# Performance work log

Hardware: AMD Instinct MI355X
Metric: run time of the kernel (lower is better)

Reference implementation:

```python
import jax, jax.numpy as jnp
import numpy as np

NUM_NODES = 512

def chebyshev_convolution(laplacian, signal, weights, t0):
    # Faithful port of the torch helper, including tk_prev staying equal to
    # `laplacian` throughout the loop (as in the source).
    k = weights.shape[0]
    # t0 is the identity, so t0 @ signal == signal
    out = jnp.matmul(signal, weights[0])
    out = out + jnp.matmul(jnp.matmul(laplacian, signal), weights[1])
    tk_prev = laplacian
    tk = 2.0 * jnp.matmul(laplacian, laplacian) - t0
    for i in range(2, k):
        out = out + jnp.matmul(jnp.matmul(tk, signal), weights[i])
        tk = 2.0 * jnp.matmul(laplacian, tk) - tk_prev
    return out


def setup_inputs() -> dict:
    key = jax.random.key(0)
    ks = jax.random.split(key, 5)
    B, T, N, C_IN, C_OUT, CS, CD = 4, 12, NUM_NODES, 64, 64, 3, 6
    std_l = 0.1 / np.sqrt(N)
    std_t = 0.1 / np.sqrt(C_IN)
    x = jax.random.normal(ks[0], (B, T, N, C_IN), dtype=jnp.float32)
    ws = jax.random.uniform(ks[1], (N, N), jnp.float32, -std_l, std_l)
    ts = jax.random.uniform(ks[2], (CS, C_IN, C_OUT), jnp.float32, -std_t, std_t)
    wp = jax.random.uniform(ks[3], (C_IN, C_IN), jnp.float32, -std_t, std_t)
    td = jax.random.uniform(ks[4], (CD, C_IN, C_OUT), jnp.float32, -std_t, std_t)
    return {"x": x, "ws": ws, "ts": ts, "wp": wp, "td": td}


def reference(x, ws, ts, wp, td):
    N = NUM_NODES
    t0 = jnp.eye(N, dtype=x.dtype)
    # Static (SGC) branch: Chebyshev conv with learned static Laplacian ws
    out_s = chebyshev_convolution(ws, x, ts, t0)
    # Dynamic branch: data-dependent Laplacian wd = x @ (wp @ x^T)  -> (B,T,N,N)
    wd = jnp.matmul(x, jnp.matmul(wp, jnp.swapaxes(x, -2, -1)))
    wd = wd + jnp.min(wd)
    wd = wd / jnp.max(wd) / (N ** 2)
    out_d = chebyshev_convolution(wd, x, td, t0)
    return out_s + out_d
```

## Files before the change

### kernel.cpp

```cpp
#include <hip/hip_runtime.h>
#include <cstddef>
#include <cstdint>

#define NN 512
#define CC 64
#define BT 48

typedef __bf16 bf16_t;
typedef bf16_t bf16x8 __attribute__((ext_vector_type(8)));
typedef bf16_t bf16x4 __attribute__((ext_vector_type(4)));
typedef float f32x4 __attribute__((ext_vector_type(4)));

#define OFF_MN    0
#define OFF_MX    384
#define OFF_WSB   1024
#define OFF_WS2B  132096
#define OFF_XBT   263168
#define OFF_XNB   1049600
#define OFF_XNR   1836032
#define OFF_CS0   2622464
#define OFF_T1T   2647040
#define OFF_T2T   2649088
#define OFF_Z1N   2651136
#define OFF_Z2N   3437568
#define OFF_WEB   4224000
#define OFF_WER   4322304
#define OFF_VDY   4420608

__device__ __forceinline__ f32x4 mfma(bf16x8 a, bf16x8 b, f32x4 c) {
  return __builtin_amdgcn_mfma_f32_16x16x32_bf16(a, b, c, 0, 0, 0);
}
__device__ __forceinline__ int swz_chunk(int r, int c8) {
  return r * 64 + ((c8 ^ (r & 7)) << 3);
}
__device__ __forceinline__ int swz_e(int r, int c) {
  return r * 64 + ((((c >> 3) ^ (r & 7)) << 3)) + (c & 7);
}
__device__ __forceinline__ bf16x8 frag(const bf16_t* sm, int row, int kc) {
  return *(const bf16x8*)(sm + row * 64 + ((kc ^ (row & 7)) << 3));
}
__device__ __forceinline__ void stage64(bf16_t* sm, const bf16_t* g, int ld, int tid) {
#pragma unroll
  for (int j = 0; j < 2; ++j) {
    int id = tid + 256 * j;
    int r = id >> 3, c8 = id & 7;
    bf16x8 v = *(const bf16x8*)(g + (size_t)r * ld + c8 * 8);
    *(bf16x8*)(sm + swz_chunk(r, c8)) = v;
  }
}
__device__ __forceinline__ void stage64f(bf16_t* sm, const float* g, int ld, int tid) {
#pragma unroll
  for (int j = 0; j < 4; ++j) {
    int idx = tid + 256 * j;
    int r = idx >> 4, cc = (idx & 15) * 4;
    float4 v = *(const float4*)(g + (size_t)r * ld + cc);
    bf16x4 o = {(bf16_t)v.x, (bf16_t)v.y, (bf16_t)v.z, (bf16_t)v.w};
    *(bf16x4*)(sm + swz_e(r, cc)) = o;
  }
}
struct bfpair { bf16_t b, r; };
__device__ __forceinline__ bfpair splitbf(float f) {
  bfpair p;
  p.b = (bf16_t)f;
  p.r = (bf16_t)(f - (float)p.b);
  return p;
}

__global__ __launch_bounds__(256) void k_pre(
    const float* __restrict__ x, const float* __restrict__ wsL,
    const float* __restrict__ ts, const float* __restrict__ wp,
    float* __restrict__ wsf)
{
  __shared__ __align__(16) char pool[32768];
  __shared__ float red[16];
  const int tid = threadIdx.x;
  const int b = blockIdx.x;
  const int w = tid >> 6, l = tid & 63, lh = l >> 4, lr = l & 15, m0 = w * 16;

  if (b < 384) {
    const int bt = (b & 7) + 8 * (b >> 6);
    const int it = (b >> 3) & 7;
    const int i0 = it * 64;
    float (*XsF)[66] = (float(*)[66])pool;
    bf16_t* XBT = (bf16_t*)(wsf + OFF_XBT);
    bf16_t* XNb = (bf16_t*)(wsf + OFF_XNB);
    bf16_t* XNr = (bf16_t*)(wsf + OFF_XNR);
    float* CS0 = wsf + OFF_CS0;
    const float* xg = x + ((size_t)bt * NN + i0) * CC;
    for (int j = 0; j < 4; ++j) {
      int idx = tid + 256 * j;
      int r = idx >> 4, c0v = (idx & 15) * 4;
      float4 v = *(const float4*)(xg + (size_t)r * CC + c0v);
      bfpair p0 = splitbf(v.x), p1 = splitbf(v.y), p2 = splitbf(v.z), p3 = splitbf(v.w);
      bf16x4 vb = {p0.b, p1.b, p2.b, p3.b};
      bf16x4 vr = {p0.r, p1.r, p2.r, p3.r};
      size_t gb = ((size_t)bt * 512 + i0 + r) * 64 + c0v;
      *(bf16x4*)(XNb + gb) = vb;
      *(bf16x4*)(XNr + gb) = vr;
      XsF[c0v + 0][r] = v.x; XsF[c0v + 1][r] = v.y;
      XsF[c0v + 2][r] = v.z; XsF[c0v + 3][r] = v.w;
    }
    __syncthreads();
    {
      int c = tid >> 2, k0 = (tid & 3) * 16;
      bf16x8 o1, o2;
#pragma unroll
      for (int q = 0; q < 8; ++q) {
        o1[q] = (bf16_t)XsF[c][k0 + q];
        o2[q] = (bf16_t)XsF[c][k0 + 8 + q];
      }
      size_t base = ((size_t)bt * 64 + c) * 512 + i0 + k0;
      *(bf16x8*)(XBT + base) = o1; *(bf16x8*)(XBT + base + 8) = o2;
    }
    if (tid < 64) {
      float s = 0.f;
      for (int r = 0; r < 64; ++r) s += XsF[tid][r];
      CS0[((size_t)bt * 8 + it) * 64 + tid] = s;
    }
    return;
  }
  if (b < 768) {
    const int g = b - 384;
    const int bt = (g & 7) + 8 * (g >> 6);
    const int bx = (g >> 3) & 7;
    bf16_t* WpT  = (bf16_t*)pool;
    bf16_t* Xa   = (bf16_t*)(pool + 8192);
    bf16_t* Hs   = (bf16_t*)(pool + 16384);
    bf16_t* Xcol = (bf16_t*)(pool + 24576);
    for (int j = 0; j < 4; ++j) {
      int idx = tid + 256 * j;
      int r = idx >> 4, cc = (idx & 15) * 4;
      float4 v = *(const float4*)(wp + r * 64 + cc);
      WpT[swz_e(cc + 0, r)] = (bf16_t)v.x;
      WpT[swz_e(cc + 1, r)] = (bf16_t)v.y;
      WpT[swz_e(cc + 2, r)] = (bf16_t)v.z;
      WpT[swz_e(cc + 3, r)] = (bf16_t)v.w;
    }
    stage64f(Xa, x + ((size_t)bt * NN + bx * 64) * CC, 64, tid);
    __syncthreads();
    f32x4 hacc[4] = {};
#pragma unroll
    for (int q = 0; q < 2; ++q) {
      bf16x8 a = frag(Xa, m0 + lr, q * 4 + lh);
#pragma unroll
      for (int t = 0; t < 4; ++t)
        hacc[t] = mfma(a, frag(WpT, t * 16 + lr, q * 4 + lh), hacc[t]);
    }
#pragma unroll
    for (int t = 0; t < 4; ++t)
#pragma unroll
      for (int r_ = 0; r_ < 4; ++r_)
        Hs[swz_e(m0 + 4 * lh + r_, t * 16 + lr)] = (bf16_t)hacc[t][r_];
    float mn = 3.4e38f, mx = -3.4e38f;
    for (int byj = 0; byj < 8; ++byj) {
      __syncthreads();
      stage64f(Xcol, x + ((size_t)bt * NN + byj * 64) * CC, 64, tid);
      __syncthreads();
      f32x4 acc[4] = {};
#pragma unroll
      for (int q = 0; q < 2; ++q) {
        bf16x8 a = frag(Hs, m0 + lr, q * 4 + lh);
#pragma unroll
        for (int t = 0; t < 4; ++t)
          acc[t] = mfma(a, frag(Xcol, t * 16 + lr, q * 4 + lh), acc[t]);
      }
#pragma unroll
      for (int t = 0; t < 4; ++t)
#pragma unroll
        for (int r_ = 0; r_ < 4; ++r_) {
          mn = fminf(mn, acc[t][r_]); mx = fmaxf(mx, acc[t][r_]);
        }
    }
    for (int off = 32; off; off >>= 1) {
      mn = fminf(mn, __shfl_xor(mn, off));
      mx = fmaxf(mx, __shfl_xor(mx, off));
    }
    if (l == 0) { red[w] = mn; red[8 + w] = mx; }
    __syncthreads();
    if (tid == 0) {
      mn = fminf(fminf(red[0], red[1]), fminf(red[2], red[3]));
      mx = fmaxf(fmaxf(red[8], red[9]), fmaxf(red[10], red[11]));
      wsf[OFF_MN + g] = mn; wsf[OFF_MX + g] = mx;
    }
    return;
  }
  if (b < 832) {
    const int idx2 = b - 768;
    bf16_t* Asb = (bf16_t*)pool;
    bf16_t* Bsb = (bf16_t*)(pool + 8192);
    bf16_t* Ys  = (bf16_t*)(pool + 16384);
    bf16_t* WS2B = (bf16_t*)(wsf + OFF_WS2B);
    const int r0 = (idx2 >> 3) * 64, c0 = (idx2 & 7) * 64;
    f32x4 acc[4] = {};
    for (int jj = 0; jj < 8; ++jj) {
      if (jj) __syncthreads();
      for (int j = 0; j < 4; ++j) {
        int idx = tid + 256 * j;
        int r = idx >> 4, cc = (idx & 15) * 4;
        float4 v = *(const float4*)(wsL + (size_t)(r0 + r) * 512 + jj * 64 + cc);
        bf16x4 vb = {(bf16_t)v.x, (bf16_t)v.y, (bf16_t)v.z, (bf16_t)v.w};
        *(bf16x4*)(Asb + swz_e(r, cc)) = vb;
        float4 u = *(const float4*)(wsL + (size_t)(jj * 64 + r) * 512 + c0 + cc);
        Bsb[swz_e(cc + 0, r)] = (bf16_t)u.x;
        Bsb[swz_e(cc + 1, r)] = (bf16_t)u.y;
        Bsb[swz_e(cc + 2, r)] = (bf16_t)u.z;
        Bsb[swz_e(cc + 3, r)] = (bf16_t)u.w;
      }
      __syncthreads();
#pragma unroll
      for (int q = 0; q < 2; ++q) {
        bf16x8 a = frag(Asb, m0 + lr, q * 4 + lh);
#pragma unroll
        for (int t = 0; t < 4; ++t)
          acc[t] = mfma(a, frag(Bsb, t * 16 + lr, q * 4 + lh), acc[t]);
      }
    }
#pragma unroll
    for (int t = 0; t < 4; ++t)
#pragma unroll
      for (int r_ = 0; r_ < 4; ++r_) {
        int row = m0 + 4 * lh + r_, col = t * 16 + lr;
        float v = 2.0f * acc[t][r_] - ((r0 + row) == (c0 + col) ? 1.0f : 0.0f);
        Ys[swz_e(row, col)] = (bf16_t)v;
      }
    __syncthreads();
#pragma unroll
    for (int j = 0; j < 2; ++j) {
      int id = tid + 256 * j;
      int r = id >> 3, c8 = id & 7;
      *(bf16x8*)(WS2B + (size_t)(r0 + r) * 512 + c0 + c8 * 8) =
          *(const bf16x8*)(Ys + swz_chunk(r, c8));
    }
    return;
  }
  if (b < 840) {
    const int bx = b - 832;
    const float* wrow = wsL + (size_t)bx * 64 * 512;
    bf16_t* wob = (bf16_t*)(wsf + OFF_WSB) + (size_t)bx * 64 * 512;
    for (int j = 0; j < 32; ++j) {
      int idx = tid + 256 * j;
      float4 v = *(const float4*)(wrow + (size_t)idx * 4);
      bf16x4 o = {(bf16_t)v.x, (bf16_t)v.y, (bf16_t)v.z, (bf16_t)v.w};
      *(bf16x4*)(wob + (size_t)idx * 4) = o;
    }
    return;
  }
  {
    bf16_t* T1 = (bf16_t*)(wsf + OFF_T1T);
    bf16_t* T2 = (bf16_t*)(wsf + OFF_T2T);
    const float* t1g = ts + 4096;
    const float* t2g = ts + 8192;
    for (int j = 0; j < 16; ++j) {
      int idx = tid + 256 * j;
      int cin = idx >> 6, co = idx & 63;
      T1[co * 64 + cin] = (bf16_t)t1g[cin * 64 + co];
      T2[co * 64 + cin] = (bf16_t)t2g[cin * 64 + co];
    }
  }
}

__global__ __launch_bounds__(256) void k_mix(
    const float* __restrict__ ts, const float* __restrict__ wp,
    const float* __restrict__ td, float* __restrict__ wsf)
{
  __shared__ __align__(16) char pool[66688];
  const int tid = threadIdx.x;
  const int bid = blockIdx.x;
  const int w = tid >> 6, l = tid & 63, lh = l >> 4, lr = l & 15, m0 = w * 16;

  if (bid >= 48) {
    const int g = bid - 48;
    const int bt = (g & 7) + 8 * (g >> 6);
    const int n0 = ((g >> 3) & 7) * 64;
    bf16_t* As = (bf16_t*)pool;
    bf16_t* B1 = (bf16_t*)(pool + 8192);
    bf16_t* B2 = (bf16_t*)(pool + 16384);
    const bf16_t* XBT = (const bf16_t*)(wsf + OFF_XBT);
    const bf16_t* WSB = (const bf16_t*)(wsf + OFF_WSB);
    const bf16_t* WS2B = (const bf16_t*)(wsf + OFF_WS2B);
    f32x4 acc1[4] = {}, acc2[4] = {};
    for (int kk = 0; kk < 8; ++kk) {
      if (kk) __syncthreads();
      stage64(As, XBT + (size_t)bt * 32768 + kk * 64, 512, tid);
      stage64(B1, WSB + (size_t)n0 * 512 + kk * 64, 512, tid);
      stage64(B2, WS2B + (size_t)n0 * 512 + kk * 64, 512, tid);
      __syncthreads();
#pragma unroll
      for (int q = 0; q < 2; ++q) {
        bf16x8 a = frag(As, m0 + lr, q * 4 + lh);
#pragma unroll
        for (int t = 0; t < 4; ++t) {
          acc1[t] = mfma(a, frag(B1, t * 16 + lr, q * 4 + lh), acc1[t]);
          acc2[t] = mfma(a, frag(B2, t * 16 + lr, q * 4 + lh), acc2[t]);
        }
      }
    }
    __syncthreads();
#pragma unroll
    for (int t = 0; t < 4; ++t)
#pragma unroll
      for (int r_ = 0; r_ < 4; ++r_) {
        int cy = m0 + 4 * lh + r_, nl = t * 16 + lr;
        As[swz_e(nl, cy)] = (bf16_t)acc1[t][r_];
        B1[swz_e(nl, cy)] = (bf16_t)acc2[t][r_];
      }
    __syncthreads();
    bf16_t* Z1N = (bf16_t*)(wsf + OFF_Z1N);
    bf16_t* Z2N = (bf16_t*)(wsf + OFF_Z2N);
#pragma unroll
    for (int j = 0; j < 2; ++j) {
      int id = tid + 256 * j;
      int r = id >> 3, c8 = id & 7;
      size_t gb = ((size_t)bt * 512 + n0 + r) * 64 + c8 * 8;
      *(bf16x8*)(Z1N + gb) = *(const bf16x8*)(As + swz_chunk(r, c8));
      *(bf16x8*)(Z2N + gb) = *(const bf16x8*)(B1 + swz_chunk(r, c8));
    }
    return;
  }
  const int bt = bid;
  bf16_t* XB  = (bf16_t*)pool;
  bf16_t* Ab0 = (bf16_t*)pool;
  bf16_t* AT0 = (bf16_t*)(pool + 8192);
  bf16_t* Ab1 = (bf16_t*)(pool + 16384);
  bf16_t* AT1 = (bf16_t*)(pool + 24576);
  bf16_t* Gb  = (bf16_t*)(pool + 32768);
  bf16_t* WpT = (bf16_t*)(pool + 40960);
  bf16_t* tdA = (bf16_t*)(pool + 49152);
  bf16_t* tdB = (bf16_t*)(pool + 57344);
  float* vec = (float*)(pool + 65536);
  float* uF = vec;        float* hF = vec + 64;
  float* b0 = vec + 128;  float* b1 = vec + 192;
  float* redv = vec + 256;
  const bf16_t* XBTg = (const bf16_t*)(wsf + OFF_XBT);
  const float* CS0 = wsf + OFF_CS0;
  for (int kk = 0; kk < 8; ++kk)
    stage64(XB + kk * 4096, XBTg + (size_t)bt * 32768 + kk * 64, 512, tid);
  {
    float mn = 3.4e38f, mx = -3.4e38f;
    for (int i = tid; i < 384; i += 256) {
      mn = fminf(mn, wsf[OFF_MN + i]);
      mx = fmaxf(mx, wsf[OFF_MX + i]);
    }
    for (int off = 32; off; off >>= 1) {
      mn = fminf(mn, __shfl_xor(mn, off));
      mx = fmaxf(mx, __shfl_xor(mx, off));
    }
    if (l == 0) { redv[w] = mn; redv[8 + w] = mx; }
  }
  if (tid < 64) {
    float s = 0.f;
#pragma unroll
    for (int p = 0; p < 8; ++p) s += CS0[((size_t)bt * 8 + p) * 64 + tid];
    uF[tid] = s; b0[tid] = s;
  }
  __syncthreads();
  f32x4 pacc[4] = {};
  for (int kk = 0; kk < 8; ++kk) {
    const bf16_t* xt = XB + kk * 4096;
#pragma unroll
    for (int q = 0; q < 2; ++q) {
      bf16x8 a = frag(xt, m0 + lr, q * 4 + lh);
#pragma unroll
      for (int t = 0; t < 4; ++t)
        pacc[t] = mfma(a, frag(xt, t * 16 + lr, q * 4 + lh), pacc[t]);
    }
  }
  const float mnA = fminf(fminf(redv[0], redv[1]), fminf(redv[2], redv[3]));
  const float mxA = fmaxf(fmaxf(redv[8], redv[9]), fmaxf(redv[10], redv[11]));
  const float s_sc = 1.0f / (mxA + mnA) / 262144.0f;
  const float c_sc = mnA * s_sc;
  __syncthreads();
#pragma unroll
  for (int t = 0; t < 4; ++t)
#pragma unroll
    for (int r_ = 0; r_ < 4; ++r_) {
      int m = m0 + 4 * lh + r_, jc = t * 16 + lr;
      bf16_t bv = (bf16_t)pacc[t][r_];
      Ab0[swz_e(m, jc)] = bv; AT0[swz_e(jc, m)] = bv;
    }
  for (int j = 0; j < 4; ++j) {
    int idx = tid + 256 * j;
    int r = idx >> 4, cc = (idx & 15) * 4;
    float4 v = *(const float4*)(wp + r * 64 + cc);
    WpT[swz_e(cc + 0, r)] = (bf16_t)v.x;
    WpT[swz_e(cc + 1, r)] = (bf16_t)v.y;
    WpT[swz_e(cc + 2, r)] = (bf16_t)v.z;
    WpT[swz_e(cc + 3, r)] = (bf16_t)v.w;
  }
  for (int j = 0; j < 4; ++j) {
    int idx = tid + 256 * j;
    int cin = idx >> 4, co = (idx & 15) * 4;
    float4 v = *(const float4*)(td + 4096 + cin * 64 + co);
    tdA[swz_e(co + 0, cin)] = (bf16_t)v.x;
    tdA[swz_e(co + 1, cin)] = (bf16_t)v.y;
    tdA[swz_e(co + 2, cin)] = (bf16_t)v.z;
    tdA[swz_e(co + 3, cin)] = (bf16_t)v.w;
  }
  __syncthreads();
  {
    int jj = tid >> 2, sub = tid & 3;
    float s = 0.f;
    for (int c = sub * 16; c < sub * 16 + 16; ++c)
      s += (float)WpT[swz_e(jj, c)] * uF[c];
    s += __shfl_xor(s, 1); s += __shfl_xor(s, 2);
    if (sub == 0) hF[jj] = s;
  }
  {
    f32x4 gv[4] = {};
#pragma unroll
    for (int q = 0; q < 2; ++q) {
      bf16x8 a = frag(Ab0, m0 + lr, q * 4 + lh);
#pragma unroll
      for (int t = 0; t < 4; ++t)
        gv[t] = mfma(a, frag(WpT, t * 16 + lr, q * 4 + lh), gv[t]);
    }
#pragma unroll
    for (int t = 0; t < 4; ++t)
#pragma unroll
      for (int r_ = 0; r_ < 4; ++r_)
        Gb[swz_e(m0 + 4 * lh + r_, t * 16 + lr)] = (bf16_t)gv[t][r_];
  }
  __syncthreads();
  float mu = 0.f, vacc = 0.f;
  f32x4 Macc[4] = {};
  for (int i = 1; i <= 5; ++i) {
    const float* bcur = (i & 1) ? b0 : b1;
    float* bnx = (i & 1) ? b1 : b0;
    const bf16_t* tdc = (i & 1) ? tdA : tdB;
    const bf16_t* AbC = (i & 1) ? Ab0 : Ab1;
    const bf16_t* ATC = (i & 1) ? AT0 : AT1;
    bf16_t* AbN = (i & 1) ? Ab1 : Ab0;
    bf16_t* ATN = (i & 1) ? AT1 : AT0;
    if (i < 5) {
      bf16_t* tdn = (i & 1) ? tdB : tdA;
      for (int j = 0; j < 4; ++j) {
        int idx = tid + 256 * j;
        int cin = idx >> 4, co = (idx & 15) * 4;
        float4 v = *(const float4*)(td + (i + 1) * 4096 + cin * 64 + co);
        tdn[swz_e(co + 0, cin)] = (bf16_t)v.x;
        tdn[swz_e(co + 1, cin)] = (bf16_t)v.y;
        tdn[swz_e(co + 2, cin)] = (bf16_t)v.z;
        tdn[swz_e(co + 3, cin)] = (bf16_t)v.w;
      }
    }
#pragma unroll
    for (int q = 0; q < 2; ++q) {
      bf16x8 a = frag(AbC, m0 + lr, q * 4 + lh);
#pragma unroll
      for (int t = 0; t < 4; ++t)
        Macc[t] = mfma(a, frag(tdc, t * 16 + lr, q * 4 + lh), Macc[t]);
    }
    f32x4 Aacc[4] = {};
    if (i < 5) {
#pragma unroll
      for (int q = 0; q < 2; ++q) {
        bf16x8 gfr = frag(Gb, m0 + lr, q * 4 + lh);
#pragma unroll
        for (int t = 0; t < 4; ++t)
          Aacc[t] = mfma(gfr, frag(ATC, t * 16 + lr, q * 4 + lh), Aacc[t]);
      }
    }
    {
      int co = tid >> 2, sub = tid & 3;
      float sv = 0.f;
      for (int c = sub * 16; c < sub * 16 + 16; ++c)
        sv += bcur[c] * (float)tdc[swz_e(co, c)];
      sv += __shfl_xor(sv, 1); sv += __shfl_xor(sv, 2);
      if (sub == 0) vacc += sv;
    }
    if (i < 5) {
      int jj = tid >> 2, sub = tid & 3;
      float t1 = 0.f;
      for (int m = sub * 16; m < sub * 16 + 16; ++m)
        t1 += (float)ATC[swz_e(jj, m)] * hF[m];
      t1 += __shfl_xor(t1, 1); t1 += __shfl_xor(t1, 2);
      if (sub == 0)
        bnx[jj] = 2.f * (s_sc * t1 + 512.f * c_sc * bcur[jj] + mu * uF[jj])
                  - (i >= 2 ? uF[jj] : 0.f);
    }
    if (i < 5) {
#pragma unroll
      for (int t = 0; t < 4; ++t)
#pragma unroll
        for (int r_ = 0; r_ < 4; ++r_) {
          int m = m0 + 4 * lh + r_, jc = t * 16 + lr;
          float v = 2.f * (s_sc * Aacc[t][r_] + c_sc * uF[m] * bcur[jc] + mu * pacc[t][r_])
                    - (i >= 2 ? pacc[t][r_] : 0.f);
          bf16_t bv = (bf16_t)v;
          AbN[swz_e(m, jc)] = bv; ATN[swz_e(jc, m)] = bv;
        }
      mu = (i == 1) ? -1.f : 0.f;
    }
    __syncthreads();
  }
  bf16_t* Mst = tdA;
  bf16_t* WpN = tdB;
#pragma unroll
  for (int t = 0; t < 4; ++t)
#pragma unroll
    for (int r_ = 0; r_ < 4; ++r_)
      Mst[swz_e(t * 16 + lr, m0 + 4 * lh + r_)] = (bf16_t)Macc[t][r_];
  for (int j = 0; j < 4; ++j) {
    int idx = tid + 256 * j;
    int r = idx >> 4, cc = (idx & 15) * 4;
    float4 v = *(const float4*)(wp + r * 64 + cc);
    bf16x4 o = {(bf16_t)v.x, (bf16_t)v.y, (bf16_t)v.z, (bf16_t)v.w};
    *(bf16x4*)(WpN + swz_e(r, cc)) = o;
  }
  __syncthreads();
  f32x4 wm[4] = {};
#pragma unroll
  for (int q = 0; q < 2; ++q) {
    bf16x8 a = frag(WpN, m0 + lr, q * 4 + lh);
#pragma unroll
    for (int t = 0; t < 4; ++t)
      wm[t] = mfma(a, frag(Mst, t * 16 + lr, q * 4 + lh), wm[t]);
  }
  bf16_t* WEb = (bf16_t*)(wsf + OFF_WEB);
  bf16_t* WEr = (bf16_t*)(wsf + OFF_WER);
#pragma unroll
  for (int t = 0; t < 4; ++t)
#pragma unroll
    for (int r_ = 0; r_ < 4; ++r_) {
      int a_ = m0 + 4 * lh + r_, co = t * 16 + lr;
      float weff = ts[a_ * 64 + co] + td[a_ * 64 + co] - td[2 * 4096 + a_ * 64 + co]
                   + s_sc * wm[t][r_];
      bfpair p = splitbf(weff);
      WEb[((size_t)bt * 64 + co) * 64 + a_] = p.b;
      WEr[((size_t)bt * 64 + co) * 64 + a_] = p.r;
    }
  if ((tid & 3) == 0) (wsf + OFF_VDY)[bt * 64 + (tid >> 2)] = c_sc * vacc;
}

__global__ __launch_bounds__(256) void k_epi(float* __restrict__ wsf,
                                             float* __restrict__ out)
{
  __shared__ __align__(16) bf16_t Xb[4096], Xr[4096], Z1s[4096], Z2s[4096],
                                  WEs[4096], WRs[4096], T1s[4096], T2s[4096];
  const int tid = threadIdx.x;
  const int g = blockIdx.x;
  const int bt = (g & 7) + 8 * (g >> 6);
  const int n0 = ((g >> 3) & 7) * 64;
  const int w = tid >> 6, l = tid & 63, lh = l >> 4, lr = l & 15, m0 = w * 16;
  stage64(Xb,  (const bf16_t*)(wsf + OFF_XNB) + ((size_t)bt * 512 + n0) * 64, 64, tid);
  stage64(Xr,  (const bf16_t*)(wsf + OFF_XNR) + ((size_t)bt * 512 + n0) * 64, 64, tid);
  stage64(Z1s, (const bf16_t*)(wsf + OFF_Z1N) + ((size_t)bt * 512 + n0) * 64, 64, tid);
  stage64(Z2s, (const bf16_t*)(wsf + OFF_Z2N) + ((size_t)bt * 512 + n0) * 64, 64, tid);
  stage64(WEs, (const bf16_t*)(wsf + OFF_WEB) + (size_t)bt * 4096, 64, tid);
  stage64(WRs, (const bf16_t*)(wsf + OFF_WER) + (size_t)bt * 4096, 64, tid);
  stage64(T1s, (const bf16_t*)(wsf + OFF_T1T), 64, tid);
  stage64(T2s, (const bf16_t*)(wsf + OFF_T2T), 64, tid);
  __syncthreads();
  const float* VDY = wsf + OFF_VDY;
  f32x4 accO[4];
#pragma unroll
  for (int t = 0; t < 4; ++t) {
    float vv = VDY[bt * 64 + t * 16 + lr];
    accO[t] = {vv, vv, vv, vv};
  }
#pragma unroll
  for (int q = 0; q < 2; ++q) {
    bf16x8 aXb = frag(Xb, m0 + lr, q * 4 + lh);
    bf16x8 aXr = frag(Xr, m0 + lr, q * 4 + lh);
    bf16x8 aZ1 = frag(Z1s, m0 + lr, q * 4 + lh);
    bf16x8 aZ2 = frag(Z2s, m0 + lr, q * 4 + lh);
#pragma unroll
    for (int t = 0; t < 4; ++t) {
      bf16x8 bWb = frag(WEs, t * 16 + lr, q * 4 + lh);
      bf16x8 bWr = frag(WRs, t * 16 + lr, q * 4 + lh);
      accO[t] = mfma(aXb, bWb, accO[t]);
      accO[t] = mfma(aXb, bWr, accO[t]);
      accO[t] = mfma(aXr, bWb, accO[t]);
      accO[t] = mfma(aZ1, frag(T1s, t * 16 + lr, q * 4 + lh), accO[t]);
      accO[t] = mfma(aZ2, frag(T2s, t * 16 + lr, q * 4 + lh), accO[t]);
    }
  }
#pragma unroll
  for (int t = 0; t < 4; ++t)
#pragma unroll
    for (int r_ = 0; r_ < 4; ++r_)
      out[((size_t)bt * 512 + n0 + m0 + 4 * lh + r_) * 64 + t * 16 + lr] = accO[t][r_];
}

extern "C" void kernel_launch(void* const* d_in, const int* in_sizes, int n_in,
                              void* d_out, int out_size, void* d_ws, size_t ws_size,
                              hipStream_t stream)
{
  (void)in_sizes; (void)n_in; (void)out_size; (void)ws_size;
  const float* x   = (const float*)d_in[0];
  const float* wsL = (const float*)d_in[1];
  const float* ts  = (const float*)d_in[2];
  const float* wp  = (const float*)d_in[3];
  const float* td  = (const float*)d_in[4];
  float* out = (float*)d_out;
  float* wsf = (float*)d_ws;
  dim3 b(256);

  k_pre<<<841, b, 0, stream>>>(x, wsL, ts, wp, wsf);
  k_mix<<<432, b, 0, stream>>>(ts, wp, td, wsf);
  k_epi<<<384, b, 0, stream>>>(wsf, out);
}
```

Before: 44.19 us.

## Fuse three kernels into one cooperative kernel with grid-wide syncs

Merges the preprocessing, mixing/Z-GEMM and epilogue kernels into a single persistent cooperative kernel separated by grid syncs. This removes two kernel launch boundaries. The Z1/Z2 accumulators also stay in registers across the sync, so they no longer make a global round trip. The pre stage now runs its 841 tasks in a grid-stride loop over at most 512 blocks. A fallback to the original three-launch path is used when occupancy is too low or the cooperative launch fails. The trade-off is grid-sync cost, the larger shared-memory pool possibly limiting occupancy, and extra register pressure from the live accumulators.

```diff
diff --git a/kernel.cpp b/kernel.cpp
--- a/kernel.cpp
+++ b/kernel.cpp
@@ -1,6 +1,9 @@
 #include <hip/hip_runtime.h>
+#include <hip/hip_cooperative_groups.h>
 #include <cstddef>
 #include <cstdint>
+
+namespace cg = cooperative_groups;
 
 #define NN 512
 #define CC 64
@@ -66,15 +69,12 @@
   return p;
 }
 
-__global__ __launch_bounds__(256) void k_pre(
-    const float* __restrict__ x, const float* __restrict__ wsL,
-    const float* __restrict__ ts, const float* __restrict__ wp,
-    float* __restrict__ wsf)
-{
-  __shared__ __align__(16) char pool[32768];
-  __shared__ float red[16];
-  const int tid = threadIdx.x;
-  const int b = blockIdx.x;
+__device__ void pre_task(int b, const float* __restrict__ x,
+                         const float* __restrict__ wsL,
+                         const float* __restrict__ ts,
+                         const float* __restrict__ wp,
+                         float* __restrict__ wsf, char* pool, float* red, int tid)
+{
   const int w = tid >> 6, l = tid & 63, lh = l >> 4, lr = l & 15, m0 = w * 16;
 
   if (b < 384) {
@@ -245,7 +245,7 @@
     }
     return;
   }
-  {
+  if (b == 840) {
     bf16_t* T1 = (bf16_t*)(wsf + OFF_T1T);
     bf16_t* T2 = (bf16_t*)(wsf + OFF_T2T);
     const float* t1g = ts + 4096;
@@ -259,65 +259,12 @@
   }
 }
 
-__global__ __launch_bounds__(256) void k_mix(
-    const float* __restrict__ ts, const float* __restrict__ wp,
-    const float* __restrict__ td, float* __restrict__ wsf)
-{
-  __shared__ __align__(16) char pool[66688];
-  const int tid = threadIdx.x;
-  const int bid = blockIdx.x;
+__device__ void dyn_task(int bt, const float* __restrict__ ts,
+                         const float* __restrict__ wp,
+                         const float* __restrict__ td,
+                         float* __restrict__ wsf, char* pool, int tid)
+{
   const int w = tid >> 6, l = tid & 63, lh = l >> 4, lr = l & 15, m0 = w * 16;
-
-  if (bid >= 48) {
-    const int g = bid - 48;
-    const int bt = (g & 7) + 8 * (g >> 6);
-    const int n0 = ((g >> 3) & 7) * 64;
-    bf16_t* As = (bf16_t*)pool;
-    bf16_t* B1 = (bf16_t*)(pool + 8192);
-    bf16_t* B2 = (bf16_t*)(pool + 16384);
-    const bf16_t* XBT = (const bf16_t*)(wsf + OFF_XBT);
-    const bf16_t* WSB = (const bf16_t*)(wsf + OFF_WSB);
-    const bf16_t* WS2B = (const bf16_t*)(wsf + OFF_WS2B);
-    f32x4 acc1[4] = {}, acc2[4] = {};
-    for (int kk = 0; kk < 8; ++kk) {
-      if (kk) __syncthreads();
-      stage64(As, XBT + (size_t)bt * 32768 + kk * 64, 512, tid);
-      stage64(B1, WSB + (size_t)n0 * 512 + kk * 64, 512, tid);
-      stage64(B2, WS2B + (size_t)n0 * 512 + kk * 64, 512, tid);
-      __syncthreads();
-#pragma unroll
-      for (int q = 0; q < 2; ++q) {
-        bf16x8 a = frag(As, m0 + lr, q * 4 + lh);
-#pragma unroll
-        for (int t = 0; t < 4; ++t) {
-          acc1[t] = mfma(a, frag(B1, t * 16 + lr, q * 4 + lh), acc1[t]);
-          acc2[t] = mfma(a, frag(B2, t * 16 + lr, q * 4 + lh), acc2[t]);
-        }
-      }
-    }
-    __syncthreads();
-#pragma unroll
-    for (int t = 0; t < 4; ++t)
-#pragma unroll
-      for (int r_ = 0; r_ < 4; ++r_) {
-        int cy = m0 + 4 * lh + r_, nl = t * 16 + lr;
-        As[swz_e(nl, cy)] = (bf16_t)acc1[t][r_];
-        B1[swz_e(nl, cy)] = (bf16_t)acc2[t][r_];
-      }
-    __syncthreads();
-    bf16_t* Z1N = (bf16_t*)(wsf + OFF_Z1N);
-    bf16_t* Z2N = (bf16_t*)(wsf + OFF_Z2N);
-#pragma unroll
-    for (int j = 0; j < 2; ++j) {
-      int id = tid + 256 * j;
-      int r = id >> 3, c8 = id & 7;
-      size_t gb = ((size_t)bt * 512 + n0 + r) * 64 + c8 * 8;
-      *(bf16x8*)(Z1N + gb) = *(const bf16x8*)(As + swz_chunk(r, c8));
-      *(bf16x8*)(Z2N + gb) = *(const bf16x8*)(B1 + swz_chunk(r, c8));
-    }
-    return;
-  }
-  const int bt = bid;
   bf16_t* XB  = (bf16_t*)pool;
   bf16_t* Ab0 = (bf16_t*)pool;
   bf16_t* AT0 = (bf16_t*)(pool + 8192);
@@ -532,20 +479,66 @@
   if ((tid & 3) == 0) (wsf + OFF_VDY)[bt * 64 + (tid >> 2)] = c_sc * vacc;
 }
 
-__global__ __launch_bounds__(256) void k_epi(float* __restrict__ wsf,
-                                             float* __restrict__ out)
-{
-  __shared__ __align__(16) bf16_t Xb[4096], Xr[4096], Z1s[4096], Z2s[4096],
-                                  WEs[4096], WRs[4096], T1s[4096], T2s[4096];
-  const int tid = threadIdx.x;
-  const int g = blockIdx.x;
+__device__ void zgemm_task(int g, const float* __restrict__ wsf, char* pool, int tid,
+                           f32x4 (&acc1)[4], f32x4 (&acc2)[4])
+{
+  const int w = tid >> 6, l = tid & 63, lh = l >> 4, lr = l & 15, m0 = w * 16;
   const int bt = (g & 7) + 8 * (g >> 6);
   const int n0 = ((g >> 3) & 7) * 64;
+  bf16_t* As = (bf16_t*)pool;
+  bf16_t* B1 = (bf16_t*)(pool + 8192);
+  bf16_t* B2 = (bf16_t*)(pool + 16384);
+  const bf16_t* XBT = (const bf16_t*)(wsf + OFF_XBT);
+  const bf16_t* WSB = (const bf16_t*)(wsf + OFF_WSB);
+  const bf16_t* WS2B = (const bf16_t*)(wsf + OFF_WS2B);
+  for (int kk = 0; kk < 8; ++kk) {
+    if (kk) __syncthreads();
+    stage64(As, XBT + (size_t)bt * 32768 + kk * 64, 512, tid);
+    stage64(B1, WSB + (size_t)n0 * 512 + kk * 64, 512, tid);
+    stage64(B2, WS2B + (size_t)n0 * 512 + kk * 64, 512, tid);
+    __syncthreads();
+#pragma unroll
+    for (int q = 0; q < 2; ++q) {
+      bf16x8 a = frag(As, m0 + lr, q * 4 + lh);
+#pragma unroll
+      for (int t = 0; t < 4; ++t) {
+        acc1[t] = mfma(a, frag(B1, t * 16 + lr, q * 4 + lh), acc1[t]);
+        acc2[t] = mfma(a, frag(B2, t * 16 + lr, q * 4 + lh), acc2[t]);
+      }
+    }
+  }
+}
+
+__device__ void epi_task(int g, float* __restrict__ wsf, float* __restrict__ out,
+                         char* pool, int tid,
+                         const f32x4 (&acc1)[4], const f32x4 (&acc2)[4], bool zreg)
+{
   const int w = tid >> 6, l = tid & 63, lh = l >> 4, lr = l & 15, m0 = w * 16;
+  const int bt = (g & 7) + 8 * (g >> 6);
+  const int n0 = ((g >> 3) & 7) * 64;
+  bf16_t* Xb  = (bf16_t*)pool;
+  bf16_t* Xr  = (bf16_t*)(pool + 8192);
+  bf16_t* Z1s = (bf16_t*)(pool + 16384);
+  bf16_t* Z2s = (bf16_t*)(pool + 24576);
+  bf16_t* WEs = (bf16_t*)(pool + 32768);
+  bf16_t* WRs = (bf16_t*)(pool + 40960);
+  bf16_t* T1s = (bf16_t*)(pool + 49152);
+  bf16_t* T2s = (bf16_t*)(pool + 57344);
+  if (zreg) {
+#pragma unroll
+    for (int t = 0; t < 4; ++t)
+#pragma unroll
+      for (int r_ = 0; r_ < 4; ++r_) {
+        int cy = m0 + 4 * lh + r_, nl = t * 16 + lr;
+        Z1s[swz_e(nl, cy)] = (bf16_t)acc1[t][r_];
+        Z2s[swz_e(nl, cy)] = (bf16_t)acc2[t][r_];
+      }
+  } else {
+    stage64(Z1s, (const bf16_t*)(wsf + OFF_Z1N) + ((size_t)bt * 512 + n0) * 64, 64, tid);
+    stage64(Z2s, (const bf16_t*)(wsf + OFF_Z2N) + ((size_t)bt * 512 + n0) * 64, 64, tid);
+  }
   stage64(Xb,  (const bf16_t*)(wsf + OFF_XNB) + ((size_t)bt * 512 + n0) * 64, 64, tid);
   stage64(Xr,  (const bf16_t*)(wsf + OFF_XNR) + ((size_t)bt * 512 + n0) * 64, 64, tid);
-  stage64(Z1s, (const bf16_t*)(wsf + OFF_Z1N) + ((size_t)bt * 512 + n0) * 64, 64, tid);
-  stage64(Z2s, (const bf16_t*)(wsf + OFF_Z2N) + ((size_t)bt * 512 + n0) * 64, 64, tid);
   stage64(WEs, (const bf16_t*)(wsf + OFF_WEB) + (size_t)bt * 4096, 64, tid);
   stage64(WRs, (const bf16_t*)(wsf + OFF_WER) + (size_t)bt * 4096, 64, tid);
   stage64(T1s, (const bf16_t*)(wsf + OFF_T1T), 64, tid);
@@ -582,6 +575,91 @@
       out[((size_t)bt * 512 + n0 + m0 + 4 * lh + r_) * 64 + t * 16 + lr] = accO[t][r_];
 }
 
+__global__ __launch_bounds__(256) void k_all(
+    const float* __restrict__ x, const float* __restrict__ wsL,
+    const float* __restrict__ ts, const float* __restrict__ wp,
+    const float* __restrict__ td, float* __restrict__ wsf,
+    float* __restrict__ out)
+{
+  __shared__ __align__(16) char pool[66688];
+  __shared__ float red[16];
+  const int tid = threadIdx.x;
+  f32x4 acc1[4] = {}, acc2[4] = {};
+  for (int b = blockIdx.x; b < 841; b += gridDim.x) {
+    pre_task(b, x, wsL, ts, wp, wsf, pool, red, tid);
+    __syncthreads();
+  }
+  cg::this_grid().sync();
+  {
+    const int b = blockIdx.x;
+    if (b < 48) dyn_task(b, ts, wp, td, wsf, pool, tid);
+    else if (b < 432) zgemm_task(b - 48, wsf, pool, tid, acc1, acc2);
+  }
+  cg::this_grid().sync();
+  {
+    const int b = blockIdx.x;
+    if (b >= 48 && b < 432)
+      epi_task(b - 48, wsf, out, pool, tid, acc1, acc2, true);
+  }
+}
+
+__global__ __launch_bounds__(256) void k_pre_f(
+    const float* __restrict__ x, const float* __restrict__ wsL,
+    const float* __restrict__ ts, const float* __restrict__ wp,
+    float* __restrict__ wsf)
+{
+  __shared__ __align__(16) char pool[32768];
+  __shared__ float red[16];
+  pre_task(blockIdx.x, x, wsL, ts, wp, wsf, pool, red, threadIdx.x);
+}
+
+__global__ __launch_bounds__(256) void k_mix_f(
+    const float* __restrict__ ts, const float* __restrict__ wp,
+    const float* __restrict__ td, float* __restrict__ wsf)
+{
+  __shared__ __align__(16) char pool[66688];
+  const int tid = threadIdx.x;
+  const int bid = blockIdx.x;
+  if (bid < 48) { dyn_task(bid, ts, wp, td, wsf, pool, tid); return; }
+  const int g = bid - 48;
+  const int bt = (g & 7) + 8 * (g >> 6);
+  const int n0 = ((g >> 3) & 7) * 64;
+  const int w = tid >> 6, l = tid & 63, lh = l >> 4, lr = l & 15, m0 = w * 16;
+  f32x4 acc1[4] = {}, acc2[4] = {};
+  zgemm_task(g, wsf, pool, tid, acc1, acc2);
+  __syncthreads();
+  bf16_t* As = (bf16_t*)pool;
+  bf16_t* B1 = (bf16_t*)(pool + 8192);
+#pragma unroll
+  for (int t = 0; t < 4; ++t)
+#pragma unroll
+    for (int r_ = 0; r_ < 4; ++r_) {
+      int cy = m0 + 4 * lh + r_, nl = t * 16 + lr;
+      As[swz_e(nl, cy)] = (bf16_t)acc1[t][r_];
+      B1[swz_e(nl, cy)] = (bf16_t)acc2[t][r_];
+    }
+  __syncthreads();
+  bf16_t* Z1N = (bf16_t*)(wsf + OFF_Z1N);
+  bf16_t* Z2N = (bf16_t*)(wsf + OFF_Z2N);
+#pragma unroll
+  for (int j = 0; j < 2; ++j) {
+    int id = tid + 256 * j;
+    int r = id >> 3, c8 = id & 7;
+    size_t gb = ((size_t)bt * 512 + n0 + r) * 64 + c8 * 8;
+    *(bf16x8*)(Z1N + gb) = *(const bf16x8*)(As + swz_chunk(r, c8));
+    *(bf16x8*)(Z2N + gb) = *(const bf16x8*)(B1 + swz_chunk(r, c8));
+  }
+  (void)l;
+}
+
+__global__ __launch_bounds__(256) void k_epi_f(float* __restrict__ wsf,
+                                               float* __restrict__ out)
+{
+  __shared__ __align__(16) char pool[66688];
+  f32x4 d1[4] = {}, d2[4] = {};
+  epi_task(blockIdx.x, wsf, out, pool, threadIdx.x, d1, d2, false);
+}
+
 extern "C" void kernel_launch(void* const* d_in, const int* in_sizes, int n_in,
                               void* d_out, int out_size, void* d_ws, size_t ws_size,
                               hipStream_t stream)
@@ -594,9 +672,23 @@
   const float* td  = (const float*)d_in[4];
   float* out = (float*)d_out;
   float* wsf = (float*)d_ws;
-  dim3 b(256);
-
-  k_pre<<<841, b, 0, stream>>>(x, wsL, ts, wp, wsf);
-  k_mix<<<432, b, 0, stream>>>(ts, wp, td, wsf);
-  k_epi<<<384, b, 0, stream>>>(wsf, out);
-}
+
+  int nb = 0;
+  hipError_t oe = hipOccupancyMaxActiveBlocksPerMultiprocessor(&nb, k_all, 256, 0);
+  int grid = (oe == hipSuccess ? nb : 0) * 256;
+  if (grid > 512) grid = 512;
+  bool done = false;
+  if (grid >= 432) {
+    void* args[] = {(void*)&x, (void*)&wsL, (void*)&ts, (void*)&wp,
+                    (void*)&td, (void*)&wsf, (void*)&out};
+    hipError_t le = hipLaunchCooperativeKernel(k_all, dim3(grid), dim3(256),
+                                               args, 0, stream);
+    done = (le == hipSuccess);
+  }
+  if (!done) {
+    dim3 b(256);
+    k_pre_f<<<841, b, 0, stream>>>(x, wsL, ts, wp, wsf);
+    k_mix_f<<<432, b, 0, stream>>>(ts, wp, td, wsf);
+    k_epi_f<<<384, b, 0, stream>>>(wsf, out);
+  }
+}
```

New measurement: 60.84 us. +37.7%, slower.

## Fuse epilogue into mix kernel with per-batch flag synchronization

Applied to the files above, without the earlier changes.

Merges the epilogue kernel into the mix kernel. The spatial-GEMM blocks keep their Z1/Z2 tiles in shared memory, then spin on a per-(b,t) flag set by the dynamic-branch blocks before loading the effective weights and computing the output. This removes one kernel launch and the global round trip for Z1N/Z2N. In exchange it relies on inter-block spin-waiting: if the flag-setting blocks 0-47 are not resident while the waiting blocks spin, the kernel can deadlock.

```diff
diff --git a/kernel.cpp b/kernel.cpp
--- a/kernel.cpp
+++ b/kernel.cpp
@@ -13,6 +13,7 @@
 
 #define OFF_MN    0
 #define OFF_MX    384
+#define OFF_FLG   800
 #define OFF_WSB   1024
 #define OFF_WS2B  132096
 #define OFF_XBT   263168
@@ -21,11 +22,9 @@
 #define OFF_CS0   2622464
 #define OFF_T1T   2647040
 #define OFF_T2T   2649088
-#define OFF_Z1N   2651136
-#define OFF_Z2N   3437568
-#define OFF_WEB   4224000
-#define OFF_WER   4322304
-#define OFF_VDY   4420608
+#define OFF_WEB   2651136
+#define OFF_WER   2749440
+#define OFF_VDY   2847744
 
 __device__ __forceinline__ f32x4 mfma(bf16x8 a, bf16x8 b, f32x4 c) {
   return __builtin_amdgcn_mfma_f32_16x16x32_bf16(a, b, c, 0, 0, 0);
@@ -256,25 +255,37 @@
       T1[co * 64 + cin] = (bf16_t)t1g[cin * 64 + co];
       T2[co * 64 + cin] = (bf16_t)t2g[cin * 64 + co];
     }
-  }
-}
-
-__global__ __launch_bounds__(256) void k_mix(
+    if (tid < 48) ((int*)(wsf + OFF_FLG))[tid] = 0;
+  }
+}
+
+__global__ __launch_bounds__(256) void k_fuse(
     const float* __restrict__ ts, const float* __restrict__ wp,
-    const float* __restrict__ td, float* __restrict__ wsf)
+    const float* __restrict__ td, float* __restrict__ wsf,
+    float* __restrict__ out)
 {
   __shared__ __align__(16) char pool[66688];
   const int tid = threadIdx.x;
   const int bid = blockIdx.x;
   const int w = tid >> 6, l = tid & 63, lh = l >> 4, lr = l & 15, m0 = w * 16;
+  int* flags = (int*)(wsf + OFF_FLG);
 
   if (bid >= 48) {
     const int g = bid - 48;
     const int bt = (g & 7) + 8 * (g >> 6);
     const int n0 = ((g >> 3) & 7) * 64;
-    bf16_t* As = (bf16_t*)pool;
-    bf16_t* B1 = (bf16_t*)(pool + 8192);
-    bf16_t* B2 = (bf16_t*)(pool + 16384);
+    bf16_t* As  = (bf16_t*)pool;
+    bf16_t* B1  = (bf16_t*)(pool + 8192);
+    bf16_t* B2  = (bf16_t*)(pool + 16384);
+    bf16_t* WRs = (bf16_t*)(pool + 24576);
+    bf16_t* Xb  = (bf16_t*)(pool + 32768);
+    bf16_t* Xr  = (bf16_t*)(pool + 40960);
+    bf16_t* T1s = (bf16_t*)(pool + 49152);
+    bf16_t* T2s = (bf16_t*)(pool + 57344);
+    stage64(Xb,  (const bf16_t*)(wsf + OFF_XNB) + ((size_t)bt * 512 + n0) * 64, 64, tid);
+    stage64(Xr,  (const bf16_t*)(wsf + OFF_XNR) + ((size_t)bt * 512 + n0) * 64, 64, tid);
+    stage64(T1s, (const bf16_t*)(wsf + OFF_T1T), 64, tid);
+    stage64(T2s, (const bf16_t*)(wsf + OFF_T2T), 64, tid);
     const bf16_t* XBT = (const bf16_t*)(wsf + OFF_XBT);
     const bf16_t* WSB = (const bf16_t*)(wsf + OFF_WSB);
     const bf16_t* WS2B = (const bf16_t*)(wsf + OFF_WS2B);
@@ -304,17 +315,44 @@
         As[swz_e(nl, cy)] = (bf16_t)acc1[t][r_];
         B1[swz_e(nl, cy)] = (bf16_t)acc2[t][r_];
       }
-    __syncthreads();
-    bf16_t* Z1N = (bf16_t*)(wsf + OFF_Z1N);
-    bf16_t* Z2N = (bf16_t*)(wsf + OFF_Z2N);
-#pragma unroll
-    for (int j = 0; j < 2; ++j) {
-      int id = tid + 256 * j;
-      int r = id >> 3, c8 = id & 7;
-      size_t gb = ((size_t)bt * 512 + n0 + r) * 64 + c8 * 8;
-      *(bf16x8*)(Z1N + gb) = *(const bf16x8*)(As + swz_chunk(r, c8));
-      *(bf16x8*)(Z2N + gb) = *(const bf16x8*)(B1 + swz_chunk(r, c8));
-    }
+    if (tid == 0) {
+      while (__hip_atomic_load(flags + bt, __ATOMIC_ACQUIRE,
+                               __HIP_MEMORY_SCOPE_AGENT) == 0)
+        __builtin_amdgcn_s_sleep(8);
+    }
+    __syncthreads();
+    stage64(B2,  (const bf16_t*)(wsf + OFF_WEB) + (size_t)bt * 4096, 64, tid);
+    stage64(WRs, (const bf16_t*)(wsf + OFF_WER) + (size_t)bt * 4096, 64, tid);
+    __syncthreads();
+    const float* VDY = wsf + OFF_VDY;
+    f32x4 accO[4];
+#pragma unroll
+    for (int t = 0; t < 4; ++t) {
+      float vv = VDY[bt * 64 + t * 16 + lr];
+      accO[t] = {vv, vv, vv, vv};
+    }
+#pragma unroll
+    for (int q = 0; q < 2; ++q) {
+      bf16x8 aXb = frag(Xb, m0 + lr, q * 4 + lh);
+      bf16x8 aXr = frag(Xr, m0 + lr, q * 4 + lh);
+      bf16x8 aZ1 = frag(As, m0 + lr, q * 4 + lh);
+      bf16x8 aZ2 = frag(B1, m0 + lr, q * 4 + lh);
+#pragma unroll
+      for (int t = 0; t < 4; ++t) {
+        bf16x8 bWb = frag(B2, t * 16 + lr, q * 4 + lh);
+        bf16x8 bWr = frag(WRs, t * 16 + lr, q * 4 + lh);
+        accO[t] = mfma(aXb, bWb, accO[t]);
+        accO[t] = mfma(aXb, bWr, accO[t]);
+        accO[t] = mfma(aXr, bWb, accO[t]);
+        accO[t] = mfma(aZ1, frag(T1s, t * 16 + lr, q * 4 + lh), accO[t]);
+        accO[t] = mfma(aZ2, frag(T2s, t * 16 + lr, q * 4 + lh), accO[t]);
+      }
+    }
+#pragma unroll
+    for (int t = 0; t < 4; ++t)
+#pragma unroll
+      for (int r_ = 0; r_ < 4; ++r_)
+        out[((size_t)bt * 512 + n0 + m0 + 4 * lh + r_) * 64 + t * 16 + lr] = accO[t][r_];
     return;
   }
   const int bt = bid;
@@ -530,56 +568,11 @@
       WEr[((size_t)bt * 64 + co) * 64 + a_] = p.r;
     }
   if ((tid & 3) == 0) (wsf + OFF_VDY)[bt * 64 + (tid >> 2)] = c_sc * vacc;
-}
-
-__global__ __launch_bounds__(256) void k_epi(float* __restrict__ wsf,
-                                             float* __restrict__ out)
-{
-  __shared__ __align__(16) bf16_t Xb[4096], Xr[4096], Z1s[4096], Z2s[4096],
-                                  WEs[4096], WRs[4096], T1s[4096], T2s[4096];
-  const int tid = threadIdx.x;
-  const int g = blockIdx.x;
-  const int bt = (g & 7) + 8 * (g >> 6);
-  const int n0 = ((g >> 3) & 7) * 64;
-  const int w = tid >> 6, l = tid & 63, lh = l >> 4, lr = l & 15, m0 = w * 16;
-  stage64(Xb,  (const bf16_t*)(wsf + OFF_XNB) + ((size_t)bt * 512 + n0) * 64, 64, tid);
-  stage64(Xr,  (const bf16_t*)(wsf + OFF_XNR) + ((size_t)bt * 512 + n0) * 64, 64, tid);
-  stage64(Z1s, (const bf16_t*)(wsf + OFF_Z1N) + ((size_t)bt * 512 + n0) * 64, 64, tid);
-  stage64(Z2s, (const bf16_t*)(wsf + OFF_Z2N) + ((size_t)bt * 512 + n0) * 64, 64, tid);
-  stage64(WEs, (const bf16_t*)(wsf + OFF_WEB) + (size_t)bt * 4096, 64, tid);
-  stage64(WRs, (const bf16_t*)(wsf + OFF_WER) + (size_t)bt * 4096, 64, tid);
-  stage64(T1s, (const bf16_t*)(wsf + OFF_T1T), 64, tid);
-  stage64(T2s, (const bf16_t*)(wsf + OFF_T2T), 64, tid);
   __syncthreads();
-  const float* VDY = wsf + OFF_VDY;
-  f32x4 accO[4];
-#pragma unroll
-  for (int t = 0; t < 4; ++t) {
-    float vv = VDY[bt * 64 + t * 16 + lr];
-    accO[t] = {vv, vv, vv, vv};
-  }
-#pragma unroll
-  for (int q = 0; q < 2; ++q) {
-    bf16x8 aXb = frag(Xb, m0 + lr, q * 4 + lh);
-    bf16x8 aXr = frag(Xr, m0 + lr, q * 4 + lh);
-    bf16x8 aZ1 = frag(Z1s, m0 + lr, q * 4 + lh);
-    bf16x8 aZ2 = frag(Z2s, m0 + lr, q * 4 + lh);
-#pragma unroll
-    for (int t = 0; t < 4; ++t) {
-      bf16x8 bWb = frag(WEs, t * 16 + lr, q * 4 + lh);
-      bf16x8 bWr = frag(WRs, t * 16 + lr, q * 4 + lh);
-      accO[t] = mfma(aXb, bWb, accO[t]);
-      accO[t] = mfma(aXb, bWr, accO[t]);
-      accO[t] = mfma(aXr, bWb, accO[t]);
-      accO[t] = mfma(aZ1, frag(T1s, t * 16 + lr, q * 4 + lh), accO[t]);
-      accO[t] = mfma(aZ2, frag(T2s, t * 16 + lr, q * 4 + lh), accO[t]);
-    }
-  }
-#pragma unroll
-  for (int t = 0; t < 4; ++t)
-#pragma unroll
-    for (int r_ = 0; r_ < 4; ++r_)
-      out[((size_t)bt * 512 + n0 + m0 + 4 * lh + r_) * 64 + t * 16 + lr] = accO[t][r_];
+  if (tid == 0) {
+    __threadfence();
+    __hip_atomic_store(flags + bt, 1, __ATOMIC_RELEASE, __HIP_MEMORY_SCOPE_AGENT);
+  }
 }
 
 extern "C" void kernel_launch(void* const* d_in, const int* in_sizes, int n_in,
@@ -596,7 +589,6 @@
   float* wsf = (float*)d_ws;
   dim3 b(256);
 
-  k_pre<<<841, b, 0, stream>>>(x, wsL, ts, wp, wsf);
-  k_mix<<<432, b, 0, stream>>>(ts, wp, td, wsf);
-  k_epi<<<384, b, 0, stream>>>(wsf, out);
-}
+  k_pre <<<841, b, 0, stream>>>(x, wsL, ts, wp, wsf);
+  k_fuse<<<432, b, 0, stream>>>(ts, wp, td, wsf, out);
+}
```

Result: slower. 70.67 us (+59.9%).
